# Kernel tuning notes

Hardware: AMD Instinct MI355X
Metric: run time of the kernel (lower is better)

The kernel has to match this reference:

```python
import jax, jax.numpy as jnp
import numpy as np

N_COARSE, N_FINE, N_EDGE, W, DEPTH = 16384, 65536, 393216, 128, 2


def _mlp_params(key, fan_in, width, out):
    k1, k2 = jax.random.split(key)
    w1 = jax.random.normal(k1, (fan_in, width), jnp.float32) / np.sqrt(fan_in)
    b1 = jnp.zeros((width,), jnp.float32)
    w2 = jax.random.normal(k2, (width, out), jnp.float32) / np.sqrt(width)
    b2 = jnp.zeros((out,), jnp.float32)
    return w1, b1, w2, b2


def setup_inputs() -> dict:
    key = jax.random.key(0)
    ks = jax.random.split(key, 16)
    v = jax.random.normal(ks[0], (N_COARSE, W), jnp.float32)
    c_skip = jax.random.normal(ks[1], (N_FINE, W), jnp.float32)
    e_skip = jax.random.normal(ks[2], (N_EDGE, W), jnp.float32)
    edge_index_skip = jax.random.randint(ks[3], (2, N_EDGE), 0, N_FINE, jnp.int32)
    batch_skip = jnp.zeros((N_FINE,), jnp.int32)  # single graph
    cluster = jax.random.randint(ks[4], (N_FINE,), 0, N_COARSE, jnp.int32)
    rel_pos = jax.random.normal(ks[5], (N_FINE, 1), jnp.float32)  # scalar rel pos (scalar_rel_pos=True)

    # unpooling FNN: (W + 1) -> W -> W
    uw1, ub1, uw2, ub2 = _mlp_params(ks[6], W + 1, W, W)
    # InteractionNetwork MLPs, stacked over DEPTH layers
    ew1 = []; eb1 = []; ew2 = []; eb2 = []
    nw1 = []; nb1 = []; nw2 = []; nb2 = []
    for i in range(DEPTH):
        a, b, c, d = _mlp_params(ks[7 + i], 3 * W, W, W)  # edge MLP: [e, v_s, v_r]
        ew1.append(a); eb1.append(b); ew2.append(c); eb2.append(d)
        a, b, c, d = _mlp_params(ks[9 + i], 2 * W, W, W)  # node MLP: [v, aggr(e)]
        nw1.append(a); nb1.append(b); nw2.append(c); nb2.append(d)
    stk = lambda xs: jnp.stack(xs, 0)
    return {
        'v': v, 'c_skip': c_skip, 'e_skip': e_skip, 'rel_pos': rel_pos,
        'unpool_w1': uw1, 'unpool_b1': ub1, 'unpool_w2': uw2, 'unpool_b2': ub2,
        'edge_w1': stk(ew1), 'edge_b1': stk(eb1), 'edge_w2': stk(ew2), 'edge_b2': stk(eb2),
        'node_w1': stk(nw1), 'node_b1': stk(nb1), 'node_w2': stk(nw2), 'node_b2': stk(nb2),
        'edge_index_skip': edge_index_skip, 'cluster': cluster, 'batch_skip': batch_skip,
    }


def _mlp(x, w1, b1, w2, b2):
    return jax.nn.selu(x @ w1 + b1) @ w2 + b2


def reference(v, c_skip, e_skip, rel_pos,
              unpool_w1, unpool_b1, unpool_w2, unpool_b2,
              edge_w1, edge_b1, edge_w2, edge_b2,
              node_w1, node_b1, node_w2, node_b2,
              edge_index_skip, cluster, batch_skip):
    # --- MeshUpMP: gather coarse features to fine nodes, mix with rel. pos. ---
    h = jnp.concatenate([v[cluster], rel_pos], axis=-1)            # [N_fine, W+1]
    v = _mlp(h, unpool_w1, unpool_b1, unpool_w2, unpool_b2)        # [N_fine, W]
    v = v + c_skip
    e = e_skip
    s, r = edge_index_skip[0], edge_index_skip[1]
    n_nodes = v.shape[0]
    # --- stacked InteractionNetwork layers (residual edge+node updates) ---
    for i in range(edge_w1.shape[0]):
        msg = jnp.concatenate([e, v[s], v[r]], axis=-1)            # [E, 3W]
        e = e + _mlp(msg, edge_w1[i], edge_b1[i], edge_w2[i], edge_b2[i])
        agg = jax.ops.segment_sum(e, r, num_segments=n_nodes)      # sum aggregation
        nin = jnp.concatenate([v, agg], axis=-1)                   # [N, 2W]
        v = v + _mlp(nin, node_w1[i], node_b1[i], node_w2[i], node_b2[i])
    return v
```

## Files before the change

### kernel.cpp

```cpp
#include <hip/hip_runtime.h>
#include <hip/hip_bf16.h>
#include <stdint.h>

#define NCOARSE 16384
#define NFINE   65536
#define NEDGE   393216

typedef __bf16 bf16;
typedef bf16 bf16x8 __attribute__((ext_vector_type(8)));
typedef bf16 bf16x4 __attribute__((ext_vector_type(4)));
typedef float f32x4 __attribute__((ext_vector_type(4)));

__device__ __forceinline__ float selu_f(float x) {
    return x > 0.f ? 1.0507009873554805f * x
                   : 1.7580993408473766f * (__expf(x) - 1.f);
}

__device__ __forceinline__ bf16x8 cvt8(f32x4 lo, f32x4 hi) {
    bf16x8 r;
    r[0] = (bf16)lo[0]; r[1] = (bf16)lo[1]; r[2] = (bf16)lo[2]; r[3] = (bf16)lo[3];
    r[4] = (bf16)hi[0]; r[5] = (bf16)hi[1]; r[6] = (bf16)hi[2]; r[7] = (bf16)hi[3];
    return r;
}

__global__ void prep_weights(const float* __restrict__ uw1, const float* __restrict__ uw2,
                             const float* __restrict__ ew1, const float* __restrict__ ew2,
                             const float* __restrict__ nw1, const float* __restrict__ nw2,
                             bf16* __restrict__ wb)
{
    int i = blockIdx.x * 256 + threadIdx.x;
    float v;
    if (i < 16384) {
        int j = i; int k = (j >> 12) * 32 + (j & 31), n = (j & 4095) >> 5;
        v = uw1[k * 128 + n];
    } else if (i < 32768) {
        int j = i - 16384; int k = (j >> 12) * 32 + (j & 31), n = (j & 4095) >> 5;
        v = uw2[k * 128 + n];
    } else if (i < 131072) {
        int j = i - 32768; int l = j / 49152; j -= l * 49152;
        int k = (j >> 12) * 32 + (j & 31), n = (j & 4095) >> 5;
        v = ew1[l * 49152 + k * 128 + n];
    } else if (i < 163840) {
        int j = i - 131072; int l = j >> 14; j &= 16383;
        int k = (j >> 12) * 32 + (j & 31), n = (j & 4095) >> 5;
        v = ew2[l * 16384 + k * 128 + n];
    } else if (i < 229376) {
        int j = i - 163840; int l = j >> 15; j &= 32767;
        int k = (j >> 12) * 32 + (j & 31), n = (j & 4095) >> 5;
        v = nw1[l * 32768 + k * 128 + n];
    } else {
        int j = i - 229376; int l = j >> 14; j &= 16383;
        int k = (j >> 12) * 32 + (j & 31), n = (j & 4095) >> 5;
        v = nw2[l * 16384 + k * 128 + n];
    }
    wb[i] = (bf16)v;
}

__global__ void hist_kernel(const int* __restrict__ ei, int* __restrict__ cnt) {
    int e = blockIdx.x * 256 + threadIdx.x;
    if (e < NEDGE) atomicAdd(&cnt[ei[NEDGE + e]], 1);
}

__global__ __launch_bounds__(1024)
void scan_kernel(const int* __restrict__ cnt, int* __restrict__ rowptr,
                 int* __restrict__ cursor) {
    __shared__ int part[1024];
    const int t = threadIdx.x;
    const int base = t * 64;
    int s = 0;
    for (int i = 0; i < 64; ++i) s += cnt[base + i];
    part[t] = s;
    __syncthreads();
    for (int off = 1; off < 1024; off <<= 1) {
        int v = (t >= off) ? part[t - off] : 0;
        __syncthreads();
        part[t] += v;
        __syncthreads();
    }
    int run = part[t] - s;
    for (int i = 0; i < 64; ++i) {
        int c = cnt[base + i];
        rowptr[base + i] = run;
        cursor[base + i] = run;
        run += c;
    }
    if (t == 1023) rowptr[65536] = run;
}

__global__ void scatter_kernel(const int* __restrict__ ei, int* __restrict__ cursor,
                               int* __restrict__ perm) {
    int e = blockIdx.x * 256 + threadIdx.x;
    if (e < NEDGE) {
        int r = ei[NEDGE + e];
        int p = atomicAdd(&cursor[r], 1);
        perm[p] = e;
    }
}

__global__ __launch_bounds__(256)
void agg_kernel(const bf16* __restrict__ e, const int* __restrict__ rowptr,
                const int* __restrict__ perm, bf16* __restrict__ agg) {
    int t = blockIdx.x * 256 + threadIdx.x;
    int node = t >> 3, c0 = (t & 7) * 16;
    int s = rowptr[node], en = rowptr[node + 1];
    float acc[16];
    #pragma unroll
    for (int k = 0; k < 16; ++k) acc[k] = 0.f;
    for (int j = s; j < en; ++j) {
        size_t ed = (size_t)perm[j];
        bf16x8 x0 = *(const bf16x8*)(e + ed * 128 + c0);
        bf16x8 x1 = *(const bf16x8*)(e + ed * 128 + c0 + 8);
        #pragma unroll
        for (int k = 0; k < 8; ++k) { acc[k] += (float)x0[k]; acc[8 + k] += (float)x1[k]; }
    }
    bf16x8 o0, o1;
    #pragma unroll
    for (int k = 0; k < 8; ++k) { o0[k] = (bf16)acc[k]; o1[k] = (bf16)acc[8 + k]; }
    *(bf16x8*)(agg + (size_t)node * 128 + c0) = o0;
    *(bf16x8*)(agg + (size_t)node * 128 + c0 + 8) = o1;
}

#define STAGE_LOAD2(wp0, wp1) do { \
    st0 = *(const bf16x8*)((wp0) + tid * 8); \
    st1 = *(const bf16x8*)((wp0) + 2048 + tid * 8); \
    st2 = *(const bf16x8*)((wp1) + tid * 8); \
    st3 = *(const bf16x8*)((wp1) + 2048 + tid * 8); } while (0)
#define STAGE_WRITE2(buf) do { \
    *(bf16x8*)&(buf)[0][tid >> 2][(tid & 3) * 8] = st0; \
    *(bf16x8*)&(buf)[0][(tid + 256) >> 2][(tid & 3) * 8] = st1; \
    *(bf16x8*)&(buf)[1][tid >> 2][(tid & 3) * 8] = st2; \
    *(bf16x8*)&(buf)[1][(tid + 256) >> 2][(tid & 3) * 8] = st3; } while (0)

template<bool EF32>
__global__ __launch_bounds__(256, 2)
void edge_kernel(const void* __restrict__ e_in_v,
                 bf16* __restrict__ e_out,
                 const bf16* __restrict__ v_bf,
                 const int* __restrict__ ei,
                 const bf16* __restrict__ w1s,
                 const float* __restrict__ b1,
                 const bf16* __restrict__ w2s,
                 const float* __restrict__ b2)
{
    const int tid = threadIdx.x;
    const int wv = tid >> 6, lane = tid & 63;
    const int lr = lane & 15, g = lane >> 4;
    const int wbase = blockIdx.x * 128 + wv * 32;

    __shared__ bf16 wl[2][2][128][40];
    __shared__ bf16 hid_all[4][32][136];
    bf16 (*hid)[136] = hid_all[wv];

    const float* e_f32 = (const float*)e_in_v;
    const bf16*  e_b16 = (const bf16*)e_in_v;

    int row[2], sidx[2], ridx[2];
    #pragma unroll
    for (int mt = 0; mt < 2; ++mt) {
        row[mt] = wbase + mt * 16 + lr;
        sidx[mt] = ei[row[mt]];
        ridx[mt] = ei[NEDGE + row[mt]];
    }

    bf16x8 be[4][2], bs[4][2], br[4][2];
    #pragma unroll
    for (int ks = 0; ks < 4; ++ks)
        #pragma unroll
        for (int mt = 0; mt < 2; ++mt)
            bs[ks][mt] = *(const bf16x8*)(v_bf + (size_t)sidx[mt] * 128 + ks * 32 + g * 8);
    #pragma unroll
    for (int ks = 0; ks < 4; ++ks)
        #pragma unroll
        for (int mt = 0; mt < 2; ++mt)
            br[ks][mt] = *(const bf16x8*)(v_bf + (size_t)ridx[mt] * 128 + ks * 32 + g * 8);
    if (EF32) {
        f32x4 tlo[4][2], thi[4][2];
        #pragma unroll
        for (int ks = 0; ks < 4; ++ks)
            #pragma unroll
            for (int mt = 0; mt < 2; ++mt) {
                const float* p = e_f32 + (size_t)row[mt] * 128 + ks * 32 + g * 8;
                tlo[ks][mt] = *(const f32x4*)p;
                thi[ks][mt] = *(const f32x4*)(p + 4);
            }
        #pragma unroll
        for (int ks = 0; ks < 4; ++ks)
            #pragma unroll
            for (int mt = 0; mt < 2; ++mt)
                be[ks][mt] = cvt8(tlo[ks][mt], thi[ks][mt]);
    } else {
        #pragma unroll
        for (int ks = 0; ks < 4; ++ks)
            #pragma unroll
            for (int mt = 0; mt < 2; ++mt)
                be[ks][mt] = *(const bf16x8*)(e_b16 + (size_t)row[mt] * 128 + ks * 32 + g * 8);
    }

    bf16x8 st0, st1, st2, st3;
    STAGE_LOAD2(w1s, w1s + 4096);
    STAGE_WRITE2(wl[0]);
    __syncthreads();

    f32x4 acc1[8][2], acc2[8][2];
    #pragma unroll
    for (int oc = 0; oc < 8; ++oc) {
        f32x4 z = {0.f, 0.f, 0.f, 0.f};
        acc1[oc][0] = z; acc1[oc][1] = z;
    }

    f32x4  eof[8][2];
    bf16x4 eob[8][2];

    #pragma unroll
    for (int p = 0; p < 8; ++p) {
        const int cur = p & 1;
        if (p < 7) {
            const int s0n = 2 * p + 2, s1n = 2 * p + 3;
            const bf16* wp0 = (s0n < 12) ? w1s + (size_t)s0n * 4096 : w2s + (size_t)(s0n - 12) * 4096;
            const bf16* wp1 = (s1n < 12) ? w1s + (size_t)s1n * 4096 : w2s + (size_t)(s1n - 12) * 4096;
            STAGE_LOAD2(wp0, wp1);
        }
        if (p == 6) {
            #pragma unroll
            for (int mt = 0; mt < 2; ++mt)
                #pragma unroll
                for (int oc = 0; oc < 8; ++oc) {
                    const int col = oc * 16 + g * 4;
                    if (EF32) eof[oc][mt] = *(const f32x4*)(e_f32 + (size_t)row[mt] * 128 + col);
                    else      eob[oc][mt] = *(const bf16x4*)(e_b16 + (size_t)row[mt] * 128 + col);
                }
        }
        bf16x8 a0[8], a1[8];
        #pragma unroll
        for (int oc = 0; oc < 8; ++oc) {
            a0[oc] = *(const bf16x8*)&wl[cur][0][oc * 16 + lr][g * 8];
            a1[oc] = *(const bf16x8*)&wl[cur][1][oc * 16 + lr][g * 8];
        }

        if (p < 6) {
            const int s0 = 2 * p, s1 = 2 * p + 1;
            bf16x8 b00 = (s0 < 4) ? be[s0][0] : (s0 < 8) ? bs[s0 - 4][0] : br[s0 - 8][0];
            bf16x8 b01 = (s0 < 4) ? be[s0][1] : (s0 < 8) ? bs[s0 - 4][1] : br[s0 - 8][1];
            bf16x8 b10 = (s1 < 4) ? be[s1][0] : (s1 < 8) ? bs[s1 - 4][0] : br[s1 - 8][0];
            bf16x8 b11 = (s1 < 4) ? be[s1][1] : (s1 < 8) ? bs[s1 - 4][1] : br[s1 - 8][1];
            #pragma unroll
            for (int oc = 0; oc < 8; ++oc) {
                acc1[oc][0] = __builtin_amdgcn_mfma_f32_16x16x32_bf16(a0[oc], b00, acc1[oc][0], 0, 0, 0);
                acc1[oc][1] = __builtin_amdgcn_mfma_f32_16x16x32_bf16(a0[oc], b01, acc1[oc][1], 0, 0, 0);
            }
            #pragma unroll
            for (int oc = 0; oc < 8; ++oc) {
                acc1[oc][0] = __builtin_amdgcn_mfma_f32_16x16x32_bf16(a1[oc], b10, acc1[oc][0], 0, 0, 0);
                acc1[oc][1] = __builtin_amdgcn_mfma_f32_16x16x32_bf16(a1[oc], b11, acc1[oc][1], 0, 0, 0);
            }
        } else {
            if (p == 6) {
                #pragma unroll
                for (int oc = 0; oc < 8; ++oc) {
                    f32x4 z = {0.f, 0.f, 0.f, 0.f};
                    acc2[oc][0] = z; acc2[oc][1] = z;
                }
            }
            const int k2 = 2 * (p - 6);
            bf16x8 h00 = *(const bf16x8*)&hid[lr][k2 * 32 + g * 8];
            bf16x8 h01 = *(const bf16x8*)&hid[16 + lr][k2 * 32 + g * 8];
            bf16x8 h10 = *(const bf16x8*)&hid[lr][(k2 + 1) * 32 + g * 8];
            bf16x8 h11 = *(const bf16x8*)&hid[16 + lr][(k2 + 1) * 32 + g * 8];
            #pragma unroll
            for (int oc = 0; oc < 8; ++oc) {
                acc2[oc][0] = __builtin_amdgcn_mfma_f32_16x16x32_bf16(a0[oc], h00, acc2[oc][0], 0, 0, 0);
                acc2[oc][1] = __builtin_amdgcn_mfma_f32_16x16x32_bf16(a0[oc], h01, acc2[oc][1], 0, 0, 0);
            }
            #pragma unroll
            for (int oc = 0; oc < 8; ++oc) {
                acc2[oc][0] = __builtin_amdgcn_mfma_f32_16x16x32_bf16(a1[oc], h10, acc2[oc][0], 0, 0, 0);
                acc2[oc][1] = __builtin_amdgcn_mfma_f32_16x16x32_bf16(a1[oc], h11, acc2[oc][1], 0, 0, 0);
            }
        }
        if (p == 5) {
            #pragma unroll
            for (int mt = 0; mt < 2; ++mt)
                #pragma unroll
                for (int oc = 0; oc < 8; ++oc) {
                    const int col = oc * 16 + g * 4;
                    f32x4 bv = *(const f32x4*)(b1 + col);
                    bf16x4 h;
                    #pragma unroll
                    for (int j = 0; j < 4; ++j)
                        h[j] = (bf16)selu_f(acc1[oc][mt][j] + bv[j]);
                    *(bf16x4*)&hid[mt * 16 + lr][col] = h;
                }
        }
        if (p < 7) STAGE_WRITE2(wl[cur ^ 1]);
        __syncthreads();
    }

    #pragma unroll
    for (int mt = 0; mt < 2; ++mt) {
        const size_t r = row[mt];
        #pragma unroll
        for (int oc = 0; oc < 8; ++oc) {
            const int col = oc * 16 + g * 4;
            f32x4 b2v = *(const f32x4*)(b2 + col);
            bf16x4 stv;
            #pragma unroll
            for (int j = 0; j < 4; ++j) {
                float eo = EF32 ? eof[oc][mt][j] : (float)eob[oc][mt][j];
                stv[j] = (bf16)(eo + acc2[oc][mt][j] + b2v[j]);
            }
            __builtin_nontemporal_store(stv, (bf16x4*)(e_out + r * 128 + col));
        }
    }
}

#define STAGE_LOAD(wp, st0, st1) do { \
    st0 = *(const bf16x8*)((wp) + tid * 8); \
    st1 = *(const bf16x8*)((wp) + 2048 + tid * 8); } while (0)
#define STAGE_WRITE(buf, st0, st1) do { \
    *(bf16x8*)&(buf)[tid >> 2][(tid & 3) * 8] = st0; \
    *(bf16x8*)&(buf)[(tid + 256) >> 2][(tid & 3) * 8] = st1; } while (0)

__global__ __launch_bounds__(256, 2)
void node_kernel(float* __restrict__ v_io,
                 bf16* __restrict__ v_bf,
                 const bf16* __restrict__ agg,
                 const bf16* __restrict__ w1s,
                 const float* __restrict__ b1,
                 const bf16* __restrict__ w2s,
                 const float* __restrict__ b2)
{
    const int tid = threadIdx.x;
    const int wv = tid >> 6, lane = tid & 63;
    const int lr = lane & 15, g = lane >> 4;
    const int wbase = blockIdx.x * 128 + wv * 32;

    __shared__ bf16 wl[2][128][40];
    __shared__ bf16 hid_all[4][32][136];
    bf16 (*hid)[136] = hid_all[wv];

    int row[2];
    row[0] = wbase + lr; row[1] = wbase + 16 + lr;

    bf16x8 bv[4][2], ba[4][2];
    #pragma unroll
    for (int ks = 0; ks < 4; ++ks)
        #pragma unroll
        for (int mt = 0; mt < 2; ++mt)
            bv[ks][mt] = *(const bf16x8*)(v_bf + (size_t)row[mt] * 128 + ks * 32 + g * 8);
    #pragma unroll
    for (int ks = 0; ks < 4; ++ks)
        #pragma unroll
        for (int mt = 0; mt < 2; ++mt)
            ba[ks][mt] = *(const bf16x8*)(agg + (size_t)row[mt] * 128 + ks * 32 + g * 8);

    bf16x8 st0, st1;
    STAGE_LOAD(w1s, st0, st1);
    STAGE_WRITE(wl[0], st0, st1);
    __syncthreads();

    f32x4 acc1[8][2], acc2[8][2], vo[8][2];
    #pragma unroll
    for (int oc = 0; oc < 8; ++oc) {
        f32x4 z = {0.f, 0.f, 0.f, 0.f};
        acc1[oc][0] = z; acc1[oc][1] = z;
    }

    #pragma unroll
    for (int s = 0; s < 12; ++s) {
        const int cur = s & 1;
        if (s < 11) {
            const bf16* wp = (s + 1 < 8) ? w1s + (size_t)(s + 1) * 4096
                                         : w2s + (size_t)(s + 1 - 8) * 4096;
            STAGE_LOAD(wp, st0, st1);
        }
        if (s == 8) {
            #pragma unroll
            for (int mt = 0; mt < 2; ++mt)
                #pragma unroll
                for (int oc = 0; oc < 8; ++oc)
                    vo[oc][mt] = *(const f32x4*)(v_io + (size_t)row[mt] * 128 + oc * 16 + g * 4);
        }
        bf16x8 a[8];
        #pragma unroll
        for (int oc = 0; oc < 8; ++oc)
            a[oc] = *(const bf16x8*)&wl[cur][oc * 16 + lr][g * 8];

        if (s < 8) {
            bf16x8 b0 = (s < 4) ? bv[s][0] : ba[s - 4][0];
            bf16x8 b1f = (s < 4) ? bv[s][1] : ba[s - 4][1];
            #pragma unroll
            for (int oc = 0; oc < 8; ++oc) {
                acc1[oc][0] = __builtin_amdgcn_mfma_f32_16x16x32_bf16(a[oc], b0, acc1[oc][0], 0, 0, 0);
                acc1[oc][1] = __builtin_amdgcn_mfma_f32_16x16x32_bf16(a[oc], b1f, acc1[oc][1], 0, 0, 0);
            }
        } else {
            if (s == 8) {
                #pragma unroll
                for (int oc = 0; oc < 8; ++oc) {
                    f32x4 z = {0.f, 0.f, 0.f, 0.f};
                    acc2[oc][0] = z; acc2[oc][1] = z;
                }
            }
            bf16x8 h0 = *(const bf16x8*)&hid[lr][(s - 8) * 32 + g * 8];
            bf16x8 h1 = *(const bf16x8*)&hid[16 + lr][(s - 8) * 32 + g * 8];
            #pragma unroll
            for (int oc = 0; oc < 8; ++oc) {
                acc2[oc][0] = __builtin_amdgcn_mfma_f32_16x16x32_bf16(a[oc], h0, acc2[oc][0], 0, 0, 0);
                acc2[oc][1] = __builtin_amdgcn_mfma_f32_16x16x32_bf16(a[oc], h1, acc2[oc][1], 0, 0, 0);
            }
        }
        if (s == 7) {
            #pragma unroll
            for (int mt = 0; mt < 2; ++mt)
                #pragma unroll
                for (int oc = 0; oc < 8; ++oc) {
                    const int col = oc * 16 + g * 4;
                    f32x4 bvv = *(const f32x4*)(b1 + col);
                    bf16x4 h;
                    #pragma unroll
                    for (int j = 0; j < 4; ++j)
                        h[j] = (bf16)selu_f(acc1[oc][mt][j] + bvv[j]);
                    *(bf16x4*)&hid[mt * 16 + lr][col] = h;
                }
        }
        if (s < 11) STAGE_WRITE(wl[cur ^ 1], st0, st1);
        __syncthreads();
    }

    #pragma unroll
    for (int mt = 0; mt < 2; ++mt) {
        const size_t r = row[mt];
        #pragma unroll
        for (int oc = 0; oc < 8; ++oc) {
            const int col = oc * 16 + g * 4;
            f32x4 b2v = *(const f32x4*)(b2 + col);
            f32x4 vn; bf16x4 m;
            #pragma unroll
            for (int j = 0; j < 4; ++j) {
                vn[j] = vo[oc][mt][j] + acc2[oc][mt][j] + b2v[j];
                m[j] = (bf16)vn[j];
            }
            *(f32x4*)(v_io + r * 128 + col) = vn;
            *(bf16x4*)(v_bf + r * 128 + col) = m;
        }
    }
}

__global__ __launch_bounds__(256, 2)
void unpool_kernel(const float* __restrict__ v_coarse,
                   const float* __restrict__ c_skip,
                   const float* __restrict__ rel_pos,
                   const float* __restrict__ uw1,
                   const float* __restrict__ b1,
                   const bf16* __restrict__ w1s,
                   const bf16* __restrict__ w2s,
                   const float* __restrict__ b2,
                   const int* __restrict__ cluster,
                   float* __restrict__ v_out,
                   bf16* __restrict__ v_bf)
{
    const int tid = threadIdx.x;
    const int wv = tid >> 6, lane = tid & 63;
    const int lr = lane & 15, g = lane >> 4;
    const int wbase = blockIdx.x * 128 + wv * 32;

    __shared__ bf16 wl[2][128][40];
    __shared__ bf16 hid_all[4][32][136];
    bf16 (*hid)[136] = hid_all[wv];

    int row[2], cl[2]; float relv[2];
    #pragma unroll
    for (int mt = 0; mt < 2; ++mt) {
        row[mt] = wbase + mt * 16 + lr;
        cl[mt] = cluster[row[mt]];
        relv[mt] = rel_pos[row[mt]];
    }

    bf16x8 bfr[4][2];
    {
        f32x4 tlo[4][2], thi[4][2];
        #pragma unroll
        for (int ks = 0; ks < 4; ++ks)
            #pragma unroll
            for (int mt = 0; mt < 2; ++mt) {
                const float* p = v_coarse + (size_t)cl[mt] * 128 + ks * 32 + g * 8;
                tlo[ks][mt] = *(const f32x4*)p;
                thi[ks][mt] = *(const f32x4*)(p + 4);
            }
        #pragma unroll
        for (int ks = 0; ks < 4; ++ks)
            #pragma unroll
            for (int mt = 0; mt < 2; ++mt)
                bfr[ks][mt] = cvt8(tlo[ks][mt], thi[ks][mt]);
    }

    bf16x8 st0, st1;
    STAGE_LOAD(w1s, st0, st1);
    STAGE_WRITE(wl[0], st0, st1);
    __syncthreads();

    f32x4 acc1[8][2], acc2[8][2], cs[8][2];
    #pragma unroll
    for (int oc = 0; oc < 8; ++oc) {
        f32x4 z = {0.f, 0.f, 0.f, 0.f};
        acc1[oc][0] = z; acc1[oc][1] = z;
    }

    #pragma unroll
    for (int s = 0; s < 8; ++s) {
        const int cur = s & 1;
        if (s < 7) {
            const bf16* wp = (s + 1 < 4) ? w1s + (size_t)(s + 1) * 4096
                                         : w2s + (size_t)(s + 1 - 4) * 4096;
            STAGE_LOAD(wp, st0, st1);
        }
        if (s == 4) {
            #pragma unroll
            for (int mt = 0; mt < 2; ++mt)
                #pragma unroll
                for (int oc = 0; oc < 8; ++oc)
                    cs[oc][mt] = *(const f32x4*)(c_skip + (size_t)row[mt] * 128 + oc * 16 + g * 4);
        }
        bf16x8 a[8];
        #pragma unroll
        for (int oc = 0; oc < 8; ++oc)
            a[oc] = *(const bf16x8*)&wl[cur][oc * 16 + lr][g * 8];

        if (s < 4) {
            #pragma unroll
            for (int oc = 0; oc < 8; ++oc) {
                acc1[oc][0] = __builtin_amdgcn_mfma_f32_16x16x32_bf16(a[oc], bfr[s][0], acc1[oc][0], 0, 0, 0);
                acc1[oc][1] = __builtin_amdgcn_mfma_f32_16x16x32_bf16(a[oc], bfr[s][1], acc1[oc][1], 0, 0, 0);
            }
        } else {
            if (s == 4) {
                #pragma unroll
                for (int oc = 0; oc < 8; ++oc) {
                    f32x4 z = {0.f, 0.f, 0.f, 0.f};
                    acc2[oc][0] = z; acc2[oc][1] = z;
                }
            }
            bf16x8 h0 = *(const bf16x8*)&hid[lr][(s - 4) * 32 + g * 8];
            bf16x8 h1 = *(const bf16x8*)&hid[16 + lr][(s - 4) * 32 + g * 8];
            #pragma unroll
            for (int oc = 0; oc < 8; ++oc) {
                acc2[oc][0] = __builtin_amdgcn_mfma_f32_16x16x32_bf16(a[oc], h0, acc2[oc][0], 0, 0, 0);
                acc2[oc][1] = __builtin_amdgcn_mfma_f32_16x16x32_bf16(a[oc], h1, acc2[oc][1], 0, 0, 0);
            }
        }
        if (s == 3) {
            #pragma unroll
            for (int mt = 0; mt < 2; ++mt)
                #pragma unroll
                for (int oc = 0; oc < 8; ++oc) {
                    const int col = oc * 16 + g * 4;
                    f32x4 bvv = *(const f32x4*)(b1 + col);
                    f32x4 wlr = *(const f32x4*)(uw1 + 128 * 128 + col);
                    bf16x4 h;
                    #pragma unroll
                    for (int j = 0; j < 4; ++j)
                        h[j] = (bf16)selu_f(acc1[oc][mt][j] + bvv[j] + relv[mt] * wlr[j]);
                    *(bf16x4*)&hid[mt * 16 + lr][col] = h;
                }
        }
        if (s < 7) STAGE_WRITE(wl[cur ^ 1], st0, st1);
        __syncthreads();
    }

    #pragma unroll
    for (int mt = 0; mt < 2; ++mt) {
        const size_t r = row[mt];
        #pragma unroll
        for (int oc = 0; oc < 8; ++oc) {
            const int col = oc * 16 + g * 4;
            f32x4 b2v = *(const f32x4*)(b2 + col);
            f32x4 vn; bf16x4 m;
            #pragma unroll
            for (int j = 0; j < 4; ++j) {
                vn[j] = acc2[oc][mt][j] + b2v[j] + cs[oc][mt][j];
                m[j] = (bf16)vn[j];
            }
            *(f32x4*)(v_out + r * 128 + col) = vn;
            *(bf16x4*)(v_bf + r * 128 + col) = m;
        }
    }
}

extern "C" void kernel_launch(void* const* d_in, const int* in_sizes, int n_in,
                              void* d_out, int out_size, void* d_ws, size_t ws_size,
                              hipStream_t stream) {
    const float* v_c    = (const float*)d_in[0];
    const float* c_skip = (const float*)d_in[1];
    const float* e_skip = (const float*)d_in[2];
    const float* rel    = (const float*)d_in[3];
    const float* uw1    = (const float*)d_in[4];
    const float* ub1    = (const float*)d_in[5];
    const float* uw2    = (const float*)d_in[6];
    const float* ub2    = (const float*)d_in[7];
    const float* ew1    = (const float*)d_in[8];
    const float* eb1    = (const float*)d_in[9];
    const float* ew2    = (const float*)d_in[10];
    const float* eb2    = (const float*)d_in[11];
    const float* nw1    = (const float*)d_in[12];
    const float* nb1    = (const float*)d_in[13];
    const float* nw2    = (const float*)d_in[14];
    const float* nb2    = (const float*)d_in[15];
    const int*   ei     = (const int*)d_in[16];
    const int*   clus   = (const int*)d_in[17];

    char* ws = (char*)d_ws;
    bf16*  e_bf   = (bf16*)(ws);
    bf16*  v_bf   = (bf16*)(ws + 100663296);
    bf16*  agg    = (bf16*)(ws + 117440512);
    bf16*  wb     = (bf16*)(ws + 134217728);
    int*   cnt    = (int*) (ws + 134742016);
    int*   rowptr = (int*) (ws + 135004160);
    int*   cursor = (int*) (ws + 135266308);
    int*   perm   = (int*) (ws + 135528452);

    float* vout = (float*)d_out;

    prep_weights<<<1024, 256, 0, stream>>>(uw1, uw2, ew1, ew2, nw1, nw2, wb);
    hipMemsetAsync(cnt, 0, 262144, stream);
    hist_kernel<<<1536, 256, 0, stream>>>(ei, cnt);
    scan_kernel<<<1, 1024, 0, stream>>>(cnt, rowptr, cursor);
    scatter_kernel<<<1536, 256, 0, stream>>>(ei, cursor, perm);

    unpool_kernel<<<512, 256, 0, stream>>>(v_c, c_skip, rel, uw1, ub1,
                                           wb + 0, wb + 16384, ub2, clus, vout, v_bf);

    edge_kernel<true><<<3072, 256, 0, stream>>>((const void*)e_skip, e_bf, v_bf, ei,
                                                wb + 32768, eb1, wb + 131072, eb2);
    agg_kernel<<<2048, 256, 0, stream>>>(e_bf, rowptr, perm, agg);
    node_kernel<<<512, 256, 0, stream>>>(vout, v_bf, agg,
                                         wb + 163840, nb1, wb + 229376, nb2);

    edge_kernel<false><<<3072, 256, 0, stream>>>((const void*)e_bf, e_bf, v_bf, ei,
                                                 wb + 32768 + 49152, eb1 + 128,
                                                 wb + 131072 + 16384, eb2 + 128);
    agg_kernel<<<2048, 256, 0, stream>>>(e_bf, rowptr, perm, agg);
    node_kernel<<<512, 256, 0, stream>>>(vout, v_bf, agg,
                                         wb + 163840 + 32768, nb1 + 128, wb + 229376 + 16384, nb2 + 128);
}
```

Baseline: 520.2 us.

## Make edge kernel persistent with software-prefetched gathers for the next tile

The edge MLP kernel now launches 512 blocks, and each block walks six 128-edge tiles in a loop instead of handling a single tile. During the MFMA phases of the current tile it prefetches the next tile's edge indices, its edge features and its sender and receiver node rows. Each prefetch is placed right after the registers it overwrites have been consumed, so gather latency hides behind compute. The cost is longer-lived registers and serial tile processing inside each block, and the weights are still re-streamed through LDS for every tile.

New measurement: 700.3 us. 34.6% more time.

```diff
diff --git a/kernel.cpp b/kernel.cpp
--- a/kernel.cpp
+++ b/kernel.cpp
@@ -145,7 +145,6 @@
     const int tid = threadIdx.x;
     const int wv = tid >> 6, lane = tid & 63;
     const int lr = lane & 15, g = lane >> 4;
-    const int wbase = blockIdx.x * 128 + wv * 32;
 
     __shared__ bf16 wl[2][2][128][40];
     __shared__ bf16 hid_all[4][32][136];
@@ -154,46 +153,43 @@
     const float* e_f32 = (const float*)e_in_v;
     const bf16*  e_b16 = (const bf16*)e_in_v;
 
-    int row[2], sidx[2], ridx[2];
-    #pragma unroll
-    for (int mt = 0; mt < 2; ++mt) {
-        row[mt] = wbase + mt * 16 + lr;
-        sidx[mt] = ei[row[mt]];
-        ridx[mt] = ei[NEDGE + row[mt]];
+    int row0, row1;
+    {
+        const int base = blockIdx.x * 768 + wv * 32;
+        row0 = base + lr; row1 = base + 16 + lr;
+    }
+    {
+        int s0 = ei[row0], s1 = ei[row1];
+        int r0 = ei[NEDGE + row0], r1 = ei[NEDGE + row1];
+        (void)s0; (void)s1; (void)r0; (void)r1;
     }
 
     bf16x8 be[4][2], bs[4][2], br[4][2];
-    #pragma unroll
-    for (int ks = 0; ks < 4; ++ks)
-        #pragma unroll
-        for (int mt = 0; mt < 2; ++mt)
-            bs[ks][mt] = *(const bf16x8*)(v_bf + (size_t)sidx[mt] * 128 + ks * 32 + g * 8);
-    #pragma unroll
-    for (int ks = 0; ks < 4; ++ks)
-        #pragma unroll
-        for (int mt = 0; mt < 2; ++mt)
-            br[ks][mt] = *(const bf16x8*)(v_bf + (size_t)ridx[mt] * 128 + ks * 32 + g * 8);
-    if (EF32) {
-        f32x4 tlo[4][2], thi[4][2];
-        #pragma unroll
-        for (int ks = 0; ks < 4; ++ks)
-            #pragma unroll
-            for (int mt = 0; mt < 2; ++mt) {
-                const float* p = e_f32 + (size_t)row[mt] * 128 + ks * 32 + g * 8;
-                tlo[ks][mt] = *(const f32x4*)p;
-                thi[ks][mt] = *(const f32x4*)(p + 4);
-            }
-        #pragma unroll
-        for (int ks = 0; ks < 4; ++ks)
-            #pragma unroll
-            for (int mt = 0; mt < 2; ++mt)
-                be[ks][mt] = cvt8(tlo[ks][mt], thi[ks][mt]);
-    } else {
-        #pragma unroll
-        for (int ks = 0; ks < 4; ++ks)
-            #pragma unroll
-            for (int mt = 0; mt < 2; ++mt)
-                be[ks][mt] = *(const bf16x8*)(e_b16 + (size_t)row[mt] * 128 + ks * 32 + g * 8);
+    {
+        int s0 = ei[row0], s1 = ei[row1];
+        int r0 = ei[NEDGE + row0], r1 = ei[NEDGE + row1];
+        #pragma unroll
+        for (int ks = 0; ks < 4; ++ks) {
+            bs[ks][0] = *(const bf16x8*)(v_bf + (size_t)s0 * 128 + ks * 32 + g * 8);
+            bs[ks][1] = *(const bf16x8*)(v_bf + (size_t)s1 * 128 + ks * 32 + g * 8);
+            br[ks][0] = *(const bf16x8*)(v_bf + (size_t)r0 * 128 + ks * 32 + g * 8);
+            br[ks][1] = *(const bf16x8*)(v_bf + (size_t)r1 * 128 + ks * 32 + g * 8);
+        }
+        if (EF32) {
+            #pragma unroll
+            for (int ks = 0; ks < 4; ++ks) {
+                const float* p0 = e_f32 + (size_t)row0 * 128 + ks * 32 + g * 8;
+                const float* p1 = e_f32 + (size_t)row1 * 128 + ks * 32 + g * 8;
+                be[ks][0] = cvt8(*(const f32x4*)p0, *(const f32x4*)(p0 + 4));
+                be[ks][1] = cvt8(*(const f32x4*)p1, *(const f32x4*)(p1 + 4));
+            }
+        } else {
+            #pragma unroll
+            for (int ks = 0; ks < 4; ++ks) {
+                be[ks][0] = *(const bf16x8*)(e_b16 + (size_t)row0 * 128 + ks * 32 + g * 8);
+                be[ks][1] = *(const bf16x8*)(e_b16 + (size_t)row1 * 128 + ks * 32 + g * 8);
+            }
+        }
     }
 
     bf16x8 st0, st1, st2, st3;
@@ -201,115 +197,157 @@
     STAGE_WRITE2(wl[0]);
     __syncthreads();
 
-    f32x4 acc1[8][2], acc2[8][2];
-    #pragma unroll
-    for (int oc = 0; oc < 8; ++oc) {
-        f32x4 z = {0.f, 0.f, 0.f, 0.f};
-        acc1[oc][0] = z; acc1[oc][1] = z;
-    }
-
-    f32x4  eof[8][2];
-    bf16x4 eob[8][2];
-
-    #pragma unroll
-    for (int p = 0; p < 8; ++p) {
-        const int cur = p & 1;
-        if (p < 7) {
-            const int s0n = 2 * p + 2, s1n = 2 * p + 3;
-            const bf16* wp0 = (s0n < 12) ? w1s + (size_t)s0n * 4096 : w2s + (size_t)(s0n - 12) * 4096;
-            const bf16* wp1 = (s1n < 12) ? w1s + (size_t)s1n * 4096 : w2s + (size_t)(s1n - 12) * 4096;
-            STAGE_LOAD2(wp0, wp1);
-        }
-        if (p == 6) {
-            #pragma unroll
-            for (int mt = 0; mt < 2; ++mt)
-                #pragma unroll
-                for (int oc = 0; oc < 8; ++oc) {
-                    const int col = oc * 16 + g * 4;
-                    if (EF32) eof[oc][mt] = *(const f32x4*)(e_f32 + (size_t)row[mt] * 128 + col);
-                    else      eob[oc][mt] = *(const bf16x4*)(e_b16 + (size_t)row[mt] * 128 + col);
-                }
-        }
-        bf16x8 a0[8], a1[8];
+    #pragma clang loop unroll(disable)
+    for (int t = 0; t < 6; ++t) {
+        const bool more = (t < 5);
+        int rowN0 = 0, rowN1 = 0, sN0 = 0, sN1 = 0, rN0 = 0, rN1 = 0;
+
+        f32x4 acc1[8][2], acc2[8][2];
         #pragma unroll
         for (int oc = 0; oc < 8; ++oc) {
-            a0[oc] = *(const bf16x8*)&wl[cur][0][oc * 16 + lr][g * 8];
-            a1[oc] = *(const bf16x8*)&wl[cur][1][oc * 16 + lr][g * 8];
-        }
-
-        if (p < 6) {
-            const int s0 = 2 * p, s1 = 2 * p + 1;
-            bf16x8 b00 = (s0 < 4) ? be[s0][0] : (s0 < 8) ? bs[s0 - 4][0] : br[s0 - 8][0];
-            bf16x8 b01 = (s0 < 4) ? be[s0][1] : (s0 < 8) ? bs[s0 - 4][1] : br[s0 - 8][1];
-            bf16x8 b10 = (s1 < 4) ? be[s1][0] : (s1 < 8) ? bs[s1 - 4][0] : br[s1 - 8][0];
-            bf16x8 b11 = (s1 < 4) ? be[s1][1] : (s1 < 8) ? bs[s1 - 4][1] : br[s1 - 8][1];
+            f32x4 z = {0.f, 0.f, 0.f, 0.f};
+            acc1[oc][0] = z; acc1[oc][1] = z;
+        }
+
+        #pragma unroll
+        for (int p = 0; p < 8; ++p) {
+            const int cur = p & 1;
+            if (p < 7) {
+                const int s0n = 2 * p + 2, s1n = 2 * p + 3;
+                const bf16* wp0 = (s0n < 12) ? w1s + (size_t)s0n * 4096 : w2s + (size_t)(s0n - 12) * 4096;
+                const bf16* wp1 = (s1n < 12) ? w1s + (size_t)s1n * 4096 : w2s + (size_t)(s1n - 12) * 4096;
+                STAGE_LOAD2(wp0, wp1);
+            } else if (more) {
+                STAGE_LOAD2(w1s, w1s + 4096);
+            }
+            if (p == 1 && more) {
+                const int base = blockIdx.x * 768 + (t + 1) * 128 + wv * 32;
+                rowN0 = base + lr; rowN1 = base + 16 + lr;
+                sN0 = ei[rowN0]; sN1 = ei[rowN1];
+                rN0 = ei[NEDGE + rowN0]; rN1 = ei[NEDGE + rowN1];
+            }
+            bf16x8 a0[8], a1[8];
             #pragma unroll
             for (int oc = 0; oc < 8; ++oc) {
-                acc1[oc][0] = __builtin_amdgcn_mfma_f32_16x16x32_bf16(a0[oc], b00, acc1[oc][0], 0, 0, 0);
-                acc1[oc][1] = __builtin_amdgcn_mfma_f32_16x16x32_bf16(a0[oc], b01, acc1[oc][1], 0, 0, 0);
-            }
+                a0[oc] = *(const bf16x8*)&wl[cur][0][oc * 16 + lr][g * 8];
+                a1[oc] = *(const bf16x8*)&wl[cur][1][oc * 16 + lr][g * 8];
+            }
+
+            if (p < 6) {
+                const int sg0 = 2 * p, sg1 = 2 * p + 1;
+                bf16x8 b00 = (sg0 < 4) ? be[sg0][0] : (sg0 < 8) ? bs[sg0 - 4][0] : br[sg0 - 8][0];
+                bf16x8 b01 = (sg0 < 4) ? be[sg0][1] : (sg0 < 8) ? bs[sg0 - 4][1] : br[sg0 - 8][1];
+                bf16x8 b10 = (sg1 < 4) ? be[sg1][0] : (sg1 < 8) ? bs[sg1 - 4][0] : br[sg1 - 8][0];
+                bf16x8 b11 = (sg1 < 4) ? be[sg1][1] : (sg1 < 8) ? bs[sg1 - 4][1] : br[sg1 - 8][1];
+                #pragma unroll
+                for (int oc = 0; oc < 8; ++oc) {
+                    acc1[oc][0] = __builtin_amdgcn_mfma_f32_16x16x32_bf16(a0[oc], b00, acc1[oc][0], 0, 0, 0);
+                    acc1[oc][1] = __builtin_amdgcn_mfma_f32_16x16x32_bf16(a0[oc], b01, acc1[oc][1], 0, 0, 0);
+                }
+                #pragma unroll
+                for (int oc = 0; oc < 8; ++oc) {
+                    acc1[oc][0] = __builtin_amdgcn_mfma_f32_16x16x32_bf16(a1[oc], b10, acc1[oc][0], 0, 0, 0);
+                    acc1[oc][1] = __builtin_amdgcn_mfma_f32_16x16x32_bf16(a1[oc], b11, acc1[oc][1], 0, 0, 0);
+                }
+            } else {
+                if (p == 6) {
+                    #pragma unroll
+                    for (int oc = 0; oc < 8; ++oc) {
+                        f32x4 z = {0.f, 0.f, 0.f, 0.f};
+                        acc2[oc][0] = z; acc2[oc][1] = z;
+                    }
+                }
+                const int k2 = 2 * (p - 6);
+                bf16x8 h00 = *(const bf16x8*)&hid[lr][k2 * 32 + g * 8];
+                bf16x8 h01 = *(const bf16x8*)&hid[16 + lr][k2 * 32 + g * 8];
+                bf16x8 h10 = *(const bf16x8*)&hid[lr][(k2 + 1) * 32 + g * 8];
+                bf16x8 h11 = *(const bf16x8*)&hid[16 + lr][(k2 + 1) * 32 + g * 8];
+                #pragma unroll
+                for (int oc = 0; oc < 8; ++oc) {
+                    acc2[oc][0] = __builtin_amdgcn_mfma_f32_16x16x32_bf16(a0[oc], h00, acc2[oc][0], 0, 0, 0);
+                    acc2[oc][1] = __builtin_amdgcn_mfma_f32_16x16x32_bf16(a0[oc], h01, acc2[oc][1], 0, 0, 0);
+                }
+                #pragma unroll
+                for (int oc = 0; oc < 8; ++oc) {
+                    acc2[oc][0] = __builtin_amdgcn_mfma_f32_16x16x32_bf16(a1[oc], h10, acc2[oc][0], 0, 0, 0);
+                    acc2[oc][1] = __builtin_amdgcn_mfma_f32_16x16x32_bf16(a1[oc], h11, acc2[oc][1], 0, 0, 0);
+                }
+            }
+            if (p == 5) {
+                #pragma unroll
+                for (int mt = 0; mt < 2; ++mt)
+                    #pragma unroll
+                    for (int oc = 0; oc < 8; ++oc) {
+                        const int col = oc * 16 + g * 4;
+                        f32x4 bv = *(const f32x4*)(b1 + col);
+                        bf16x4 h;
+                        #pragma unroll
+                        for (int j = 0; j < 4; ++j)
+                            h[j] = (bf16)selu_f(acc1[oc][mt][j] + bv[j]);
+                        *(bf16x4*)&hid[mt * 16 + lr][col] = h;
+                    }
+            }
+            if (p == 2 && more) {
+                if (EF32) {
+                    #pragma unroll
+                    for (int ks = 0; ks < 4; ++ks) {
+                        const float* p0 = e_f32 + (size_t)rowN0 * 128 + ks * 32 + g * 8;
+                        const float* p1 = e_f32 + (size_t)rowN1 * 128 + ks * 32 + g * 8;
+                        be[ks][0] = cvt8(*(const f32x4*)p0, *(const f32x4*)(p0 + 4));
+                        be[ks][1] = cvt8(*(const f32x4*)p1, *(const f32x4*)(p1 + 4));
+                    }
+                } else {
+                    #pragma unroll
+                    for (int ks = 0; ks < 4; ++ks) {
+                        be[ks][0] = *(const bf16x8*)(e_b16 + (size_t)rowN0 * 128 + ks * 32 + g * 8);
+                        be[ks][1] = *(const bf16x8*)(e_b16 + (size_t)rowN1 * 128 + ks * 32 + g * 8);
+                    }
+                }
+            }
+            if (p == 4 && more) {
+                #pragma unroll
+                for (int ks = 0; ks < 4; ++ks) {
+                    bs[ks][0] = *(const bf16x8*)(v_bf + (size_t)sN0 * 128 + ks * 32 + g * 8);
+                    bs[ks][1] = *(const bf16x8*)(v_bf + (size_t)sN1 * 128 + ks * 32 + g * 8);
+                }
+            }
+            if (p == 6 && more) {
+                #pragma unroll
+                for (int ks = 0; ks < 4; ++ks) {
+                    br[ks][0] = *(const bf16x8*)(v_bf + (size_t)rN0 * 128 + ks * 32 + g * 8);
+                    br[ks][1] = *(const bf16x8*)(v_bf + (size_t)rN1 * 128 + ks * 32 + g * 8);
+                }
+            }
+            if (p < 7) STAGE_WRITE2(wl[cur ^ 1]);
+            else if (more) STAGE_WRITE2(wl[cur ^ 1]);
+            __syncthreads();
+        }
+
+        #pragma unroll
+        for (int mt = 0; mt < 2; ++mt) {
+            const size_t r = (mt == 0) ? (size_t)row0 : (size_t)row1;
+            f32x4 eof[8]; bf16x4 eob[8];
             #pragma unroll
             for (int oc = 0; oc < 8; ++oc) {
-                acc1[oc][0] = __builtin_amdgcn_mfma_f32_16x16x32_bf16(a1[oc], b10, acc1[oc][0], 0, 0, 0);
-                acc1[oc][1] = __builtin_amdgcn_mfma_f32_16x16x32_bf16(a1[oc], b11, acc1[oc][1], 0, 0, 0);
-            }
-        } else {
-            if (p == 6) {
-                #pragma unroll
-                for (int oc = 0; oc < 8; ++oc) {
-                    f32x4 z = {0.f, 0.f, 0.f, 0.f};
-                    acc2[oc][0] = z; acc2[oc][1] = z;
-                }
-            }
-            const int k2 = 2 * (p - 6);
-            bf16x8 h00 = *(const bf16x8*)&hid[lr][k2 * 32 + g * 8];
-            bf16x8 h01 = *(const bf16x8*)&hid[16 + lr][k2 * 32 + g * 8];
-            bf16x8 h10 = *(const bf16x8*)&hid[lr][(k2 + 1) * 32 + g * 8];
-            bf16x8 h11 = *(const bf16x8*)&hid[16 + lr][(k2 + 1) * 32 + g * 8];
+                const int col = oc * 16 + g * 4;
+                if (EF32) eof[oc] = *(const f32x4*)(e_f32 + r * 128 + col);
+                else      eob[oc] = *(const bf16x4*)(e_b16 + r * 128 + col);
+            }
             #pragma unroll
             for (int oc = 0; oc < 8; ++oc) {
-                acc2[oc][0] = __builtin_amdgcn_mfma_f32_16x16x32_bf16(a0[oc], h00, acc2[oc][0], 0, 0, 0);
-                acc2[oc][1] = __builtin_amdgcn_mfma_f32_16x16x32_bf16(a0[oc], h01, acc2[oc][1], 0, 0, 0);
-            }
-            #pragma unroll
-            for (int oc = 0; oc < 8; ++oc) {
-                acc2[oc][0] = __builtin_amdgcn_mfma_f32_16x16x32_bf16(a1[oc], h10, acc2[oc][0], 0, 0, 0);
-                acc2[oc][1] = __builtin_amdgcn_mfma_f32_16x16x32_bf16(a1[oc], h11, acc2[oc][1], 0, 0, 0);
-            }
-        }
-        if (p == 5) {
-            #pragma unroll
-            for (int mt = 0; mt < 2; ++mt)
-                #pragma unroll
-                for (int oc = 0; oc < 8; ++oc) {
-                    const int col = oc * 16 + g * 4;
-                    f32x4 bv = *(const f32x4*)(b1 + col);
-                    bf16x4 h;
-                    #pragma unroll
-                    for (int j = 0; j < 4; ++j)
-                        h[j] = (bf16)selu_f(acc1[oc][mt][j] + bv[j]);
-                    *(bf16x4*)&hid[mt * 16 + lr][col] = h;
-                }
-        }
-        if (p < 7) STAGE_WRITE2(wl[cur ^ 1]);
-        __syncthreads();
-    }
-
-    #pragma unroll
-    for (int mt = 0; mt < 2; ++mt) {
-        const size_t r = row[mt];
-        #pragma unroll
-        for (int oc = 0; oc < 8; ++oc) {
-            const int col = oc * 16 + g * 4;
-            f32x4 b2v = *(const f32x4*)(b2 + col);
-            bf16x4 stv;
-            #pragma unroll
-            for (int j = 0; j < 4; ++j) {
-                float eo = EF32 ? eof[oc][mt][j] : (float)eob[oc][mt][j];
-                stv[j] = (bf16)(eo + acc2[oc][mt][j] + b2v[j]);
-            }
-            __builtin_nontemporal_store(stv, (bf16x4*)(e_out + r * 128 + col));
-        }
+                const int col = oc * 16 + g * 4;
+                f32x4 b2v = *(const f32x4*)(b2 + col);
+                bf16x4 stv;
+                #pragma unroll
+                for (int j = 0; j < 4; ++j) {
+                    float eo = EF32 ? eof[oc][j] : (float)eob[oc][j];
+                    stv[j] = (bf16)(eo + acc2[oc][mt][j] + b2v[j]);
+                }
+                __builtin_nontemporal_store(stv, (bf16x4*)(e_out + r * 128 + col));
+            }
+        }
+
+        row0 = rowN0; row1 = rowN1;
     }
 }
 
@@ -629,15 +667,15 @@
     unpool_kernel<<<512, 256, 0, stream>>>(v_c, c_skip, rel, uw1, ub1,
                                            wb + 0, wb + 16384, ub2, clus, vout, v_bf);
 
-    edge_kernel<true><<<3072, 256, 0, stream>>>((const void*)e_skip, e_bf, v_bf, ei,
-                                                wb + 32768, eb1, wb + 131072, eb2);
+    edge_kernel<true><<<512, 256, 0, stream>>>((const void*)e_skip, e_bf, v_bf, ei,
+                                               wb + 32768, eb1, wb + 131072, eb2);
     agg_kernel<<<2048, 256, 0, stream>>>(e_bf, rowptr, perm, agg);
     node_kernel<<<512, 256, 0, stream>>>(vout, v_bf, agg,
                                          wb + 163840, nb1, wb + 229376, nb2);
 
-    edge_kernel<false><<<3072, 256, 0, stream>>>((const void*)e_bf, e_bf, v_bf, ei,
-                                                 wb + 32768 + 49152, eb1 + 128,
-                                                 wb + 131072 + 16384, eb2 + 128);
+    edge_kernel<false><<<512, 256, 0, stream>>>((const void*)e_bf, e_bf, v_bf, ei,
+                                                wb + 32768 + 49152, eb1 + 128,
+                                                wb + 131072 + 16384, eb2 + 128);
     agg_kernel<<<2048, 256, 0, stream>>>(e_bf, rowptr, perm, agg);
     node_kernel<<<512, 256, 0, stream>>>(vout, v_bf, agg,
                                          wb + 163840 + 32768, nb1 + 128, wb + 229376 + 16384, nb2 + 128);
```
